# Performance work log

Hardware: AMD Instinct MI355X
Metric: run time of the kernel (lower is better)

The kernel has to match this reference:

```python
import jax, jax.numpy as jnp
import numpy as np

N_NODES = 100000
N_EDGES = 600000
N_GRAPHS = 64
DIM_IN = 128


def setup_inputs() -> dict:
    key = jax.random.key(0)
    ks = jax.random.split(key, 12)
    s = 0.05
    return {
        "feat": jax.random.normal(ks[0], (N_NODES, DIM_IN), jnp.float32),
        "Wself1": jax.random.normal(ks[1], (DIM_IN, 100), jnp.float32) * s,
        "Wneigh1": jax.random.normal(ks[2], (DIM_IN, 100), jnp.float32) * s,
        "b1": jnp.zeros((100,), jnp.float32),
        "Wself2": jax.random.normal(ks[3], (100, 20), jnp.float32) * s,
        "Wneigh2": jax.random.normal(ks[4], (100, 20), jnp.float32) * s,
        "b2": jnp.zeros((20,), jnp.float32),
        "fc1_w": jax.random.normal(ks[5], (20, 10), jnp.float32) * s,
        "fc1_b": jnp.zeros((10,), jnp.float32),
        "fc2_w": jax.random.normal(ks[6], (10, 1), jnp.float32) * s,
        "fc2_b": jnp.zeros((1,), jnp.float32),
        "src": jax.random.randint(ks[7], (N_EDGES,), 0, N_NODES, jnp.int32),
        "dst": jax.random.randint(ks[8], (N_EDGES,), 0, N_NODES, jnp.int32),
        "graph_ids": jnp.sort(jax.random.randint(ks[9], (N_NODES,), 0, N_GRAPHS, jnp.int32)),
    }


def _sage_mean(x, src, dst, inv_deg, Wself, Wneigh, b):
    # DGL SAGEConv(aggr='mean'): fc_self(h) + fc_neigh(mean of in-neighbor feats)
    msg = x[src]  # [E, d] gather
    agg = jax.ops.segment_sum(msg, dst, num_segments=N_NODES) * inv_deg  # [N, d]
    return x @ Wself + agg @ Wneigh + b


def reference(feat, Wself1, Wneigh1, b1, Wself2, Wneigh2, b2,
              fc1_w, fc1_b, fc2_w, fc2_b, src, dst, graph_ids):
    ones_e = jnp.ones((src.shape[0],), feat.dtype)
    deg = jax.ops.segment_sum(ones_e, dst, num_segments=N_NODES)
    inv_deg = (1.0 / jnp.maximum(deg, 1.0))[:, None]  # zero in-degree -> agg stays 0

    h = jax.nn.relu(_sage_mean(feat, src, dst, inv_deg, Wself1, Wneigh1, b1))
    h = jax.nn.relu(_sage_mean(h, src, dst, inv_deg, Wself2, Wneigh2, b2))

    # dgl.mean_nodes: per-graph mean over nodes
    ones_n = jnp.ones((h.shape[0],), h.dtype)
    counts = jax.ops.segment_sum(ones_n, graph_ids, num_segments=N_GRAPHS)
    hg = jax.ops.segment_sum(h, graph_ids, num_segments=N_GRAPHS) / jnp.maximum(counts, 1.0)[:, None]

    out = jax.nn.relu(hg @ fc1_w + fc1_b) @ fc2_w + fc2_b  # [G, 1]
    return out
```

## Files before the change

kernel.cpp:

```cpp
#include <hip/hip_runtime.h>
#include <cstddef>

#define N_NODES  100000
#define N_EDGES  600000
#define N_GRAPHS 64

__device__ __forceinline__ void atomAddF(float* p, float v) {
    unsafeAtomicAdd(p, v);
}

typedef __attribute__((address_space(1))) void GV;
typedef __attribute__((address_space(3))) void LV;
__device__ __forceinline__ void gload16(const float* g, float* l) {
    __builtin_amdgcn_global_load_lds((GV*)g, (LV*)l, 16, 0, 0);
}

__global__ __launch_bounds__(256) void deg_count(const int* __restrict__ dst,
                                                 int* __restrict__ deg) {
    int e = blockIdx.x * 256 + threadIdx.x;
    if (e < N_EDGES) atomicAdd(deg + dst[e], 1);
}

__global__ __launch_bounds__(256)
void alloc_ranges(const int* __restrict__ deg, int* __restrict__ beg,
                  int* __restrict__ cur, int* __restrict__ counter) {
    int n = blockIdx.x * 256 + threadIdx.x;
    int d = (n < N_NODES) ? deg[n] : 0;
    int lane = threadIdx.x & 63, wid = threadIdx.x >> 6;
    int incl = d;
#pragma unroll
    for (int o = 1; o < 64; o <<= 1) {
        int v = __shfl_up(incl, o);
        if (lane >= o) incl += v;
    }
    __shared__ int wsum[4];
    __shared__ int blockBase;
    if (lane == 63) wsum[wid] = incl;
    __syncthreads();
    if (threadIdx.x == 0) {
        int tot = wsum[0] + wsum[1] + wsum[2] + wsum[3];
        blockBase = atomicAdd(counter, tot);
    }
    __syncthreads();
    int base = blockBase;
    for (int w = 0; w < wid; ++w) base += wsum[w];
    int start = base + incl - d;
    if (n < N_NODES) { beg[n] = start; cur[n] = start; }
}

__global__ __launch_bounds__(256)
void csr_fill(const int* __restrict__ src, const int* __restrict__ dst,
              int* __restrict__ cur, int* __restrict__ csr_src) {
    int e = blockIdx.x * 256 + threadIdx.x;
    if (e >= N_EDGES) return;
    int p = atomicAdd(cur + dst[e], 1);
    csr_src[p] = src[e];
}

__global__ __launch_bounds__(256, 6)
void gemm1(const float* __restrict__ feat, const float* __restrict__ Wself,
           const float* __restrict__ Wneigh,
           float* __restrict__ S1, float* __restrict__ N1) {
    __shared__ float As[40 * 16];
    __shared__ float Bs[16][200];
    const int tid  = threadIdx.x;
    const int m0   = blockIdx.x * 40;
    const int wave = tid >> 6;
    const int lane = tid & 63;
    const bool active = tid < 250;
    const int tr  = tid / 25;
    const int tcc = tid % 25;
    const int sw  = tr & 3;

    float4 acc0[4], acc1[4];
#pragma unroll
    for (int i = 0; i < 4; ++i) {
        acc0[i] = make_float4(0.f, 0.f, 0.f, 0.f);
        acc1[i] = make_float4(0.f, 0.f, 0.f, 0.f);
    }

    for (int kt = 0; kt < 8; ++kt) {
        const int k0 = kt * 16;
        if (kt) __syncthreads();

        if (lane < 40) {
            int u  = wave * 40 + lane;
            int r  = u >> 2;
            int k4 = (u & 3) ^ ((r >> 2) & 3);
            gload16(feat + (size_t)(m0 + r) * 128 + k0 + k4 * 4, &As[wave * 160]);
        }
        for (int idx = tid; idx < 800; idx += 256) {
            int k = idx / 50, n4 = idx % 50;
            int n = n4 * 4;
            int gk = k0 + k;
            float4 v;
            if (n < 100) v = *reinterpret_cast<const float4*>(Wself + gk * 100 + n);
            else         v = *reinterpret_cast<const float4*>(Wneigh + gk * 100 + (n - 100));
            *reinterpret_cast<float4*>(&Bs[k][n]) = v;
        }
        __syncthreads();

        if (active) {
            const int abase = tr * 64;
#pragma unroll 4
            for (int k = 0; k < 16; ++k) {
                const float4 b0 = *reinterpret_cast<const float4*>(&Bs[k][tcc * 4]);
                const float4 b1 = *reinterpret_cast<const float4*>(&Bs[k][100 + tcc * 4]);
                const int kc = ((k >> 2) ^ sw) * 4 + (k & 3);
#pragma unroll
                for (int i = 0; i < 4; ++i) {
                    const float a = As[abase + i * 16 + kc];
                    acc0[i].x = fmaf(a, b0.x, acc0[i].x);
                    acc0[i].y = fmaf(a, b0.y, acc0[i].y);
                    acc0[i].z = fmaf(a, b0.z, acc0[i].z);
                    acc0[i].w = fmaf(a, b0.w, acc0[i].w);
                    acc1[i].x = fmaf(a, b1.x, acc1[i].x);
                    acc1[i].y = fmaf(a, b1.y, acc1[i].y);
                    acc1[i].z = fmaf(a, b1.z, acc1[i].z);
                    acc1[i].w = fmaf(a, b1.w, acc1[i].w);
                }
            }
        }
    }

    if (active) {
        const int c = tcc * 4;
#pragma unroll
        for (int i = 0; i < 4; ++i) {
            int gr = m0 + tr * 4 + i;
            *reinterpret_cast<float4*>(S1 + (size_t)gr * 100 + c) = acc0[i];
            *reinterpret_cast<float4*>(N1 + (size_t)gr * 100 + c) = acc1[i];
        }
    }
}

__global__ __launch_bounds__(256)
void aggregate1(const float* __restrict__ N1, const int* __restrict__ csr_src,
                const int* __restrict__ beg, const int* __restrict__ cur,
                float* __restrict__ A1) {
    int n  = blockIdx.x * 8 + (threadIdx.x >> 5);
    int c4 = threadIdx.x & 31;
    if (n >= N_NODES || c4 >= 25) return;
    int b = beg[n], end = cur[n];
    float4 acc = make_float4(0.f, 0.f, 0.f, 0.f);
    int j = b;
    for (; j + 1 < end; j += 2) {
        int s0 = csr_src[j], s1 = csr_src[j + 1];
        float4 v0 = *reinterpret_cast<const float4*>(N1 + (size_t)s0 * 100 + c4 * 4);
        float4 v1 = *reinterpret_cast<const float4*>(N1 + (size_t)s1 * 100 + c4 * 4);
        acc.x += v0.x + v1.x; acc.y += v0.y + v1.y;
        acc.z += v0.z + v1.z; acc.w += v0.w + v1.w;
    }
    if (j < end) {
        int s = csr_src[j];
        float4 v = *reinterpret_cast<const float4*>(N1 + (size_t)s * 100 + c4 * 4);
        acc.x += v.x; acc.y += v.y; acc.z += v.z; acc.w += v.w;
    }
    *reinterpret_cast<float4*>(A1 + (size_t)n * 100 + c4 * 4) = acc;
}

__global__ __launch_bounds__(256)
void gemm2(const float* __restrict__ S1, const float* __restrict__ A1,
           const int* __restrict__ deg, const float* __restrict__ b1,
           const float* __restrict__ Ws2, const float* __restrict__ Wn2,
           float* __restrict__ S2, float* __restrict__ N2) {
    __shared__ float As[64][108];
    __shared__ float Bs[100][64];
    const int tid = threadIdx.x;
    const int m0  = blockIdx.x * 64;

    for (int idx = tid; idx < 100 * 16; idx += 256) {
        int k = idx >> 4, n4 = idx & 15;
        int n = n4 * 4;
        float4 v = make_float4(0.f, 0.f, 0.f, 0.f);
        if (n < 20)       v = *reinterpret_cast<const float4*>(Ws2 + k * 20 + n);
        else if (n < 40)  v = *reinterpret_cast<const float4*>(Wn2 + k * 20 + (n - 20));
        *reinterpret_cast<float4*>(&Bs[k][n]) = v;
    }
    for (int idx = tid; idx < 64 * 25; idx += 256) {
        int r = idx / 25, k4 = idx % 25;
        int gr = m0 + r;
        float4 h = make_float4(0.f, 0.f, 0.f, 0.f);
        if (gr < N_NODES) {
            float4 s  = *reinterpret_cast<const float4*>(S1 + (size_t)gr * 100 + k4 * 4);
            float4 a  = *reinterpret_cast<const float4*>(A1 + (size_t)gr * 100 + k4 * 4);
            float4 bb = *reinterpret_cast<const float4*>(b1 + k4 * 4);
            float inv = 1.0f / (float)max(deg[gr], 1);
            h.x = fmaxf(fmaf(a.x, inv, s.x) + bb.x, 0.f);
            h.y = fmaxf(fmaf(a.y, inv, s.y) + bb.y, 0.f);
            h.z = fmaxf(fmaf(a.z, inv, s.z) + bb.z, 0.f);
            h.w = fmaxf(fmaf(a.w, inv, s.w) + bb.w, 0.f);
        }
        *reinterpret_cast<float4*>(&As[r][k4 * 4]) = h;
    }
    __syncthreads();

    const int tr = tid >> 4, tc = tid & 15;
    float acc[4][4] = {};
#pragma unroll 4
    for (int k = 0; k < 100; ++k) {
        float a0 = As[tr * 4 + 0][k];
        float a1 = As[tr * 4 + 1][k];
        float a2 = As[tr * 4 + 2][k];
        float a3 = As[tr * 4 + 3][k];
        float4 b = *reinterpret_cast<const float4*>(&Bs[k][tc * 4]);
        acc[0][0] += a0 * b.x; acc[0][1] += a0 * b.y; acc[0][2] += a0 * b.z; acc[0][3] += a0 * b.w;
        acc[1][0] += a1 * b.x; acc[1][1] += a1 * b.y; acc[1][2] += a1 * b.z; acc[1][3] += a1 * b.w;
        acc[2][0] += a2 * b.x; acc[2][1] += a2 * b.y; acc[2][2] += a2 * b.z; acc[2][3] += a2 * b.w;
        acc[3][0] += a3 * b.x; acc[3][1] += a3 * b.y; acc[3][2] += a3 * b.z; acc[3][3] += a3 * b.w;
    }

#pragma unroll
    for (int i = 0; i < 4; ++i) {
        int gr = m0 + tr * 4 + i;
        if (gr >= N_NODES) continue;
        int n = tc * 4;
        float4 v = make_float4(acc[i][0], acc[i][1], acc[i][2], acc[i][3]);
        if (n < 20)       *reinterpret_cast<float4*>(S2 + (size_t)gr * 20 + n) = v;
        else if (n < 40)  *reinterpret_cast<float4*>(N2 + (size_t)gr * 20 + (n - 20)) = v;
    }
}

__global__ __launch_bounds__(256)
void aggregate2(const float* __restrict__ N2, const int* __restrict__ csr_src,
                const int* __restrict__ beg, const int* __restrict__ cur,
                float* __restrict__ A2) {
    int n  = blockIdx.x * 32 + (threadIdx.x >> 3);
    int c4 = threadIdx.x & 7;
    if (n >= N_NODES || c4 >= 5) return;
    int b = beg[n], end = cur[n];
    float4 acc = make_float4(0.f, 0.f, 0.f, 0.f);
    int j = b;
    for (; j + 1 < end; j += 2) {
        int s0 = csr_src[j], s1 = csr_src[j + 1];
        float4 v0 = *reinterpret_cast<const float4*>(N2 + (size_t)s0 * 20 + c4 * 4);
        float4 v1 = *reinterpret_cast<const float4*>(N2 + (size_t)s1 * 20 + c4 * 4);
        acc.x += v0.x + v1.x; acc.y += v0.y + v1.y;
        acc.z += v0.z + v1.z; acc.w += v0.w + v1.w;
    }
    if (j < end) {
        int s = csr_src[j];
        float4 v = *reinterpret_cast<const float4*>(N2 + (size_t)s * 20 + c4 * 4);
        acc.x += v.x; acc.y += v.y; acc.z += v.z; acc.w += v.w;
    }
    *reinterpret_cast<float4*>(A2 + (size_t)n * 20 + c4 * 4) = acc;
}

__global__ __launch_bounds__(256)
void pool_kernel(const float* __restrict__ S2, const float* __restrict__ A2,
                 const int* __restrict__ deg, const float* __restrict__ b2,
                 const int* __restrict__ gids,
                 float* __restrict__ pool, float* __restrict__ cnt) {
    int n = blockIdx.x * 256 + threadIdx.x;
    float h[20];
    int g = -1;
    if (n < N_NODES) {
        g = gids[n];
        float inv = 1.0f / (float)max(deg[n], 1);
#pragma unroll
        for (int q = 0; q < 5; ++q) {
            float4 s = *reinterpret_cast<const float4*>(S2 + (size_t)n * 20 + q * 4);
            float4 a = *reinterpret_cast<const float4*>(A2 + (size_t)n * 20 + q * 4);
            float4 bb = *reinterpret_cast<const float4*>(b2 + q * 4);
            h[q * 4 + 0] = fmaxf(fmaf(a.x, inv, s.x) + bb.x, 0.f);
            h[q * 4 + 1] = fmaxf(fmaf(a.y, inv, s.y) + bb.y, 0.f);
            h[q * 4 + 2] = fmaxf(fmaf(a.z, inv, s.z) + bb.z, 0.f);
            h[q * 4 + 3] = fmaxf(fmaf(a.w, inv, s.w) + bb.w, 0.f);
        }
    } else {
#pragma unroll
        for (int c = 0; c < 20; ++c) h[c] = 0.f;
    }
    unsigned long long act = __ballot(n < N_NODES);
    int gfirst = __shfl(g, 0);
    bool uniform = __all(g == gfirst);
    if (uniform) {
        if (gfirst >= 0) {
#pragma unroll
            for (int c = 0; c < 20; ++c)
                for (int off2 = 32; off2 > 0; off2 >>= 1)
                    h[c] += __shfl_down(h[c], off2);
            if ((threadIdx.x & 63) == 0) {
                for (int c = 0; c < 20; ++c) atomAddF(&pool[gfirst * 20 + c], h[c]);
                atomAddF(&cnt[gfirst], (float)__popcll(act));
            }
        }
    } else if (n < N_NODES) {
        for (int c = 0; c < 20; ++c) atomAddF(&pool[g * 20 + c], h[c]);
        atomAddF(&cnt[g], 1.0f);
    }
}

__global__ __launch_bounds__(64)
void head(const float* __restrict__ pool, const float* __restrict__ cnt,
          const float* __restrict__ fc1w, const float* __restrict__ fc1b,
          const float* __restrict__ fc2w, const float* __restrict__ fc2b,
          float* __restrict__ out) {
    int g = threadIdx.x;
    if (g >= N_GRAPHS) return;
    float inv = 1.0f / fmaxf(cnt[g], 1.0f);
    float hg[20];
    for (int c = 0; c < 20; ++c) hg[c] = pool[g * 20 + c] * inv;
    float o = fc2b[0];
    for (int j = 0; j < 10; ++j) {
        float t = fc1b[j];
        for (int c = 0; c < 20; ++c) t = fmaf(hg[c], fc1w[c * 10 + j], t);
        o = fmaf(fmaxf(t, 0.f), fc2w[j], o);
    }
    out[g] = o;
}

extern "C" void kernel_launch(void* const* d_in, const int* in_sizes, int n_in,
                              void* d_out, int out_size, void* d_ws, size_t ws_size,
                              hipStream_t stream) {
    const float* feat   = (const float*)d_in[0];
    const float* Wself1 = (const float*)d_in[1];
    const float* Wneigh1= (const float*)d_in[2];
    const float* b1     = (const float*)d_in[3];
    const float* Wself2 = (const float*)d_in[4];
    const float* Wneigh2= (const float*)d_in[5];
    const float* b2     = (const float*)d_in[6];
    const float* fc1w   = (const float*)d_in[7];
    const float* fc1b   = (const float*)d_in[8];
    const float* fc2w   = (const float*)d_in[9];
    const float* fc2b   = (const float*)d_in[10];
    const int*   src    = (const int*)d_in[11];
    const int*   dst    = (const int*)d_in[12];
    const int*   gids   = (const int*)d_in[13];
    float* ws = (float*)d_ws;

    float* S1 = ws;
    float* N1 = ws + 10000000;
    float* A1 = ws + 20000000;
    float* S2 = N1;
    float* N2 = N1 + 2000000;
    float* A2 = A1;
    int*   deg  = (int*)(ws + 30000000);
    float* pool = ws + 30100000;
    float* cnt  = ws + 30101280;
    int*   ctr  = (int*)(ws + 30101344);
    int*   beg  = (int*)(ws + 30101360);
    int*   cur  = (int*)(ws + 30201360);
    int*   csr  = (int*)(ws + 30301360);

    hipMemsetAsync(deg, 0, (100000 + 1280 + 64 + 16) * sizeof(float), stream);

    deg_count<<<(N_EDGES + 255) / 256, 256, 0, stream>>>(dst, deg);
    alloc_ranges<<<(N_NODES + 255) / 256, 256, 0, stream>>>(deg, beg, cur, ctr);
    csr_fill<<<(N_EDGES + 255) / 256, 256, 0, stream>>>(src, dst, cur, csr);

    gemm1<<<N_NODES / 40, 256, 0, stream>>>(feat, Wself1, Wneigh1, S1, N1);

    aggregate1<<<(N_NODES + 7) / 8, 256, 0, stream>>>(N1, csr, beg, cur, A1);

    gemm2<<<(N_NODES + 63) / 64, 256, 0, stream>>>(S1, A1, deg, b1, Wself2, Wneigh2, S2, N2);

    aggregate2<<<(N_NODES + 31) / 32, 256, 0, stream>>>(N2, csr, beg, cur, A2);

    pool_kernel<<<(N_NODES + 255) / 256, 256, 0, stream>>>(S2, A2, deg, b2, gids, pool, cnt);

    head<<<1, 64, 0, stream>>>(pool, cnt, fc1w, fc1b, fc2w, fc2b, (float*)d_out);
}
```

Measured before the change: 303.7 us.

## Fuse bias/ReLU epilogue into aggregation kernels and vectorize GEMM A-reads

Moves the mean-normalize, self-term add, bias and ReLU from gemm2 and pool_kernel into aggregate1 and aggregate2. The aggregators now write final activations h1/h2, so gemm2 reads one 100-wide array instead of S1, A1 and deg. gemm2 loads its A tile with direct global-to-LDS loads, keeps only the 40 used output columns, and idles the other threads. gemm1's inner loop now reads A with float4 LDS loads, and h2 aliases S1 to reuse workspace.

After: 296.3 us. -2.4%, faster.

```diff
diff --git a/kernel.cpp b/kernel.cpp
--- a/kernel.cpp
+++ b/kernel.cpp
@@ -7,6 +7,10 @@
 
 __device__ __forceinline__ void atomAddF(float* p, float v) {
     unsafeAtomicAdd(p, v);
+}
+
+__device__ __forceinline__ float f4get(const float4& v, int i) {
+    return i == 0 ? v.x : i == 1 ? v.y : i == 2 ? v.z : v.w;
 }
 
 typedef __attribute__((address_space(1))) void GV;
@@ -102,22 +106,36 @@
 
         if (active) {
             const int abase = tr * 64;
-#pragma unroll 4
-            for (int k = 0; k < 16; ++k) {
-                const float4 b0 = *reinterpret_cast<const float4*>(&Bs[k][tcc * 4]);
-                const float4 b1 = *reinterpret_cast<const float4*>(&Bs[k][100 + tcc * 4]);
-                const int kc = ((k >> 2) ^ sw) * 4 + (k & 3);
-#pragma unroll
-                for (int i = 0; i < 4; ++i) {
-                    const float a = As[abase + i * 16 + kc];
-                    acc0[i].x = fmaf(a, b0.x, acc0[i].x);
-                    acc0[i].y = fmaf(a, b0.y, acc0[i].y);
-                    acc0[i].z = fmaf(a, b0.z, acc0[i].z);
-                    acc0[i].w = fmaf(a, b0.w, acc0[i].w);
-                    acc1[i].x = fmaf(a, b1.x, acc1[i].x);
-                    acc1[i].y = fmaf(a, b1.y, acc1[i].y);
-                    acc1[i].z = fmaf(a, b1.z, acc1[i].z);
-                    acc1[i].w = fmaf(a, b1.w, acc1[i].w);
+#pragma unroll
+            for (int g = 0; g < 4; ++g) {
+                const int ac = ((g ^ sw) << 2);
+                const float4 a0 = *reinterpret_cast<const float4*>(&As[abase +  0 + ac]);
+                const float4 a1 = *reinterpret_cast<const float4*>(&As[abase + 16 + ac]);
+                const float4 a2 = *reinterpret_cast<const float4*>(&As[abase + 32 + ac]);
+                const float4 a3 = *reinterpret_cast<const float4*>(&As[abase + 48 + ac]);
+#pragma unroll
+                for (int kl = 0; kl < 4; ++kl) {
+                    const int k = g * 4 + kl;
+                    const float4 b0 = *reinterpret_cast<const float4*>(&Bs[k][tcc * 4]);
+                    const float4 b1 = *reinterpret_cast<const float4*>(&Bs[k][100 + tcc * 4]);
+                    const float v0 = f4get(a0, kl), v1 = f4get(a1, kl);
+                    const float v2 = f4get(a2, kl), v3 = f4get(a3, kl);
+                    acc0[0].x = fmaf(v0, b0.x, acc0[0].x); acc0[0].y = fmaf(v0, b0.y, acc0[0].y);
+                    acc0[0].z = fmaf(v0, b0.z, acc0[0].z); acc0[0].w = fmaf(v0, b0.w, acc0[0].w);
+                    acc1[0].x = fmaf(v0, b1.x, acc1[0].x); acc1[0].y = fmaf(v0, b1.y, acc1[0].y);
+                    acc1[0].z = fmaf(v0, b1.z, acc1[0].z); acc1[0].w = fmaf(v0, b1.w, acc1[0].w);
+                    acc0[1].x = fmaf(v1, b0.x, acc0[1].x); acc0[1].y = fmaf(v1, b0.y, acc0[1].y);
+                    acc0[1].z = fmaf(v1, b0.z, acc0[1].z); acc0[1].w = fmaf(v1, b0.w, acc0[1].w);
+                    acc1[1].x = fmaf(v1, b1.x, acc1[1].x); acc1[1].y = fmaf(v1, b1.y, acc1[1].y);
+                    acc1[1].z = fmaf(v1, b1.z, acc1[1].z); acc1[1].w = fmaf(v1, b1.w, acc1[1].w);
+                    acc0[2].x = fmaf(v2, b0.x, acc0[2].x); acc0[2].y = fmaf(v2, b0.y, acc0[2].y);
+                    acc0[2].z = fmaf(v2, b0.z, acc0[2].z); acc0[2].w = fmaf(v2, b0.w, acc0[2].w);
+                    acc1[2].x = fmaf(v2, b1.x, acc1[2].x); acc1[2].y = fmaf(v2, b1.y, acc1[2].y);
+                    acc1[2].z = fmaf(v2, b1.z, acc1[2].z); acc1[2].w = fmaf(v2, b1.w, acc1[2].w);
+                    acc0[3].x = fmaf(v3, b0.x, acc0[3].x); acc0[3].y = fmaf(v3, b0.y, acc0[3].y);
+                    acc0[3].z = fmaf(v3, b0.z, acc0[3].z); acc0[3].w = fmaf(v3, b0.w, acc0[3].w);
+                    acc1[3].x = fmaf(v3, b1.x, acc1[3].x); acc1[3].y = fmaf(v3, b1.y, acc1[3].y);
+                    acc1[3].z = fmaf(v3, b1.z, acc1[3].z); acc1[3].w = fmaf(v3, b1.w, acc1[3].w);
                 }
             }
         }
@@ -135,9 +153,10 @@
 }
 
 __global__ __launch_bounds__(256)
-void aggregate1(const float* __restrict__ N1, const int* __restrict__ csr_src,
+void aggregate1(const float* __restrict__ N1, const float* __restrict__ S1,
+                const float* __restrict__ b1, const int* __restrict__ csr_src,
                 const int* __restrict__ beg, const int* __restrict__ cur,
-                float* __restrict__ A1) {
+                float* __restrict__ h1) {
     int n  = blockIdx.x * 8 + (threadIdx.x >> 5);
     int c4 = threadIdx.x & 31;
     if (n >= N_NODES || c4 >= 25) return;
@@ -156,75 +175,80 @@
         float4 v = *reinterpret_cast<const float4*>(N1 + (size_t)s * 100 + c4 * 4);
         acc.x += v.x; acc.y += v.y; acc.z += v.z; acc.w += v.w;
     }
-    *reinterpret_cast<float4*>(A1 + (size_t)n * 100 + c4 * 4) = acc;
-}
-
-__global__ __launch_bounds__(256)
-void gemm2(const float* __restrict__ S1, const float* __restrict__ A1,
-           const int* __restrict__ deg, const float* __restrict__ b1,
+    float inv = 1.0f / (float)max(end - b, 1);
+    float4 s  = *reinterpret_cast<const float4*>(S1 + (size_t)n * 100 + c4 * 4);
+    float4 bb = *reinterpret_cast<const float4*>(b1 + c4 * 4);
+    float4 h;
+    h.x = fmaxf(fmaf(acc.x, inv, s.x) + bb.x, 0.f);
+    h.y = fmaxf(fmaf(acc.y, inv, s.y) + bb.y, 0.f);
+    h.z = fmaxf(fmaf(acc.z, inv, s.z) + bb.z, 0.f);
+    h.w = fmaxf(fmaf(acc.w, inv, s.w) + bb.w, 0.f);
+    *reinterpret_cast<float4*>(h1 + (size_t)n * 100 + c4 * 4) = h;
+}
+
+__global__ __launch_bounds__(256)
+void gemm2(const float* __restrict__ h1,
            const float* __restrict__ Ws2, const float* __restrict__ Wn2,
            float* __restrict__ S2, float* __restrict__ N2) {
-    __shared__ float As[64][108];
-    __shared__ float Bs[100][64];
-    const int tid = threadIdx.x;
-    const int m0  = blockIdx.x * 64;
-
-    for (int idx = tid; idx < 100 * 16; idx += 256) {
-        int k = idx >> 4, n4 = idx & 15;
+    __shared__ float As[64 * 100];
+    __shared__ float Bs[100][40];
+    const int tid  = threadIdx.x;
+    const int m0   = blockIdx.x * 64;
+    const int wave = tid >> 6;
+    const int lane = tid & 63;
+
+#pragma unroll
+    for (int t = 0; t < 7; ++t) {
+        int u0 = t * 256 + wave * 64;
+        if (u0 < 1600) {
+            int u  = u0 + lane;
+            int r  = u / 25, c4 = u % 25;
+            int gr = m0 + r; if (gr >= N_NODES) gr = N_NODES - 1;
+            gload16(h1 + (size_t)gr * 100 + c4 * 4, &As[u0 * 4]);
+        }
+    }
+    for (int idx = tid; idx < 1000; idx += 256) {
+        int k = idx / 10, n4 = idx % 10;
         int n = n4 * 4;
-        float4 v = make_float4(0.f, 0.f, 0.f, 0.f);
-        if (n < 20)       v = *reinterpret_cast<const float4*>(Ws2 + k * 20 + n);
-        else if (n < 40)  v = *reinterpret_cast<const float4*>(Wn2 + k * 20 + (n - 20));
+        float4 v;
+        if (n < 20) v = *reinterpret_cast<const float4*>(Ws2 + k * 20 + n);
+        else        v = *reinterpret_cast<const float4*>(Wn2 + k * 20 + (n - 20));
         *reinterpret_cast<float4*>(&Bs[k][n]) = v;
     }
-    for (int idx = tid; idx < 64 * 25; idx += 256) {
-        int r = idx / 25, k4 = idx % 25;
-        int gr = m0 + r;
-        float4 h = make_float4(0.f, 0.f, 0.f, 0.f);
-        if (gr < N_NODES) {
-            float4 s  = *reinterpret_cast<const float4*>(S1 + (size_t)gr * 100 + k4 * 4);
-            float4 a  = *reinterpret_cast<const float4*>(A1 + (size_t)gr * 100 + k4 * 4);
-            float4 bb = *reinterpret_cast<const float4*>(b1 + k4 * 4);
-            float inv = 1.0f / (float)max(deg[gr], 1);
-            h.x = fmaxf(fmaf(a.x, inv, s.x) + bb.x, 0.f);
-            h.y = fmaxf(fmaf(a.y, inv, s.y) + bb.y, 0.f);
-            h.z = fmaxf(fmaf(a.z, inv, s.z) + bb.z, 0.f);
-            h.w = fmaxf(fmaf(a.w, inv, s.w) + bb.w, 0.f);
-        }
-        *reinterpret_cast<float4*>(&As[r][k4 * 4]) = h;
-    }
     __syncthreads();
 
     const int tr = tid >> 4, tc = tid & 15;
-    float acc[4][4] = {};
+    if (tc < 10) {
+        float acc[4][4] = {};
 #pragma unroll 4
-    for (int k = 0; k < 100; ++k) {
-        float a0 = As[tr * 4 + 0][k];
-        float a1 = As[tr * 4 + 1][k];
-        float a2 = As[tr * 4 + 2][k];
-        float a3 = As[tr * 4 + 3][k];
-        float4 b = *reinterpret_cast<const float4*>(&Bs[k][tc * 4]);
-        acc[0][0] += a0 * b.x; acc[0][1] += a0 * b.y; acc[0][2] += a0 * b.z; acc[0][3] += a0 * b.w;
-        acc[1][0] += a1 * b.x; acc[1][1] += a1 * b.y; acc[1][2] += a1 * b.z; acc[1][3] += a1 * b.w;
-        acc[2][0] += a2 * b.x; acc[2][1] += a2 * b.y; acc[2][2] += a2 * b.z; acc[2][3] += a2 * b.w;
-        acc[3][0] += a3 * b.x; acc[3][1] += a3 * b.y; acc[3][2] += a3 * b.z; acc[3][3] += a3 * b.w;
-    }
-
-#pragma unroll
-    for (int i = 0; i < 4; ++i) {
-        int gr = m0 + tr * 4 + i;
-        if (gr >= N_NODES) continue;
-        int n = tc * 4;
-        float4 v = make_float4(acc[i][0], acc[i][1], acc[i][2], acc[i][3]);
-        if (n < 20)       *reinterpret_cast<float4*>(S2 + (size_t)gr * 20 + n) = v;
-        else if (n < 40)  *reinterpret_cast<float4*>(N2 + (size_t)gr * 20 + (n - 20)) = v;
-    }
-}
-
-__global__ __launch_bounds__(256)
-void aggregate2(const float* __restrict__ N2, const int* __restrict__ csr_src,
+        for (int k = 0; k < 100; ++k) {
+            float a0 = As[(tr * 4 + 0) * 100 + k];
+            float a1 = As[(tr * 4 + 1) * 100 + k];
+            float a2 = As[(tr * 4 + 2) * 100 + k];
+            float a3 = As[(tr * 4 + 3) * 100 + k];
+            float4 b = *reinterpret_cast<const float4*>(&Bs[k][tc * 4]);
+            acc[0][0] += a0 * b.x; acc[0][1] += a0 * b.y; acc[0][2] += a0 * b.z; acc[0][3] += a0 * b.w;
+            acc[1][0] += a1 * b.x; acc[1][1] += a1 * b.y; acc[1][2] += a1 * b.z; acc[1][3] += a1 * b.w;
+            acc[2][0] += a2 * b.x; acc[2][1] += a2 * b.y; acc[2][2] += a2 * b.z; acc[2][3] += a2 * b.w;
+            acc[3][0] += a3 * b.x; acc[3][1] += a3 * b.y; acc[3][2] += a3 * b.z; acc[3][3] += a3 * b.w;
+        }
+#pragma unroll
+        for (int i = 0; i < 4; ++i) {
+            int gr = m0 + tr * 4 + i;
+            if (gr >= N_NODES) continue;
+            int n = tc * 4;
+            float4 v = make_float4(acc[i][0], acc[i][1], acc[i][2], acc[i][3]);
+            if (n < 20) *reinterpret_cast<float4*>(S2 + (size_t)gr * 20 + n) = v;
+            else        *reinterpret_cast<float4*>(N2 + (size_t)gr * 20 + (n - 20)) = v;
+        }
+    }
+}
+
+__global__ __launch_bounds__(256)
+void aggregate2(const float* __restrict__ N2, const float* __restrict__ S2,
+                const float* __restrict__ b2, const int* __restrict__ csr_src,
                 const int* __restrict__ beg, const int* __restrict__ cur,
-                float* __restrict__ A2) {
+                float* __restrict__ h2) {
     int n  = blockIdx.x * 32 + (threadIdx.x >> 3);
     int c4 = threadIdx.x & 7;
     if (n >= N_NODES || c4 >= 5) return;
@@ -243,29 +267,30 @@
         float4 v = *reinterpret_cast<const float4*>(N2 + (size_t)s * 20 + c4 * 4);
         acc.x += v.x; acc.y += v.y; acc.z += v.z; acc.w += v.w;
     }
-    *reinterpret_cast<float4*>(A2 + (size_t)n * 20 + c4 * 4) = acc;
-}
-
-__global__ __launch_bounds__(256)
-void pool_kernel(const float* __restrict__ S2, const float* __restrict__ A2,
-                 const int* __restrict__ deg, const float* __restrict__ b2,
-                 const int* __restrict__ gids,
+    float inv = 1.0f / (float)max(end - b, 1);
+    float4 s  = *reinterpret_cast<const float4*>(S2 + (size_t)n * 20 + c4 * 4);
+    float4 bb = *reinterpret_cast<const float4*>(b2 + c4 * 4);
+    float4 h;
+    h.x = fmaxf(fmaf(acc.x, inv, s.x) + bb.x, 0.f);
+    h.y = fmaxf(fmaf(acc.y, inv, s.y) + bb.y, 0.f);
+    h.z = fmaxf(fmaf(acc.z, inv, s.z) + bb.z, 0.f);
+    h.w = fmaxf(fmaf(acc.w, inv, s.w) + bb.w, 0.f);
+    *reinterpret_cast<float4*>(h2 + (size_t)n * 20 + c4 * 4) = h;
+}
+
+__global__ __launch_bounds__(256)
+void pool_kernel(const float* __restrict__ h2, const int* __restrict__ gids,
                  float* __restrict__ pool, float* __restrict__ cnt) {
     int n = blockIdx.x * 256 + threadIdx.x;
     float h[20];
     int g = -1;
     if (n < N_NODES) {
         g = gids[n];
-        float inv = 1.0f / (float)max(deg[n], 1);
 #pragma unroll
         for (int q = 0; q < 5; ++q) {
-            float4 s = *reinterpret_cast<const float4*>(S2 + (size_t)n * 20 + q * 4);
-            float4 a = *reinterpret_cast<const float4*>(A2 + (size_t)n * 20 + q * 4);
-            float4 bb = *reinterpret_cast<const float4*>(b2 + q * 4);
-            h[q * 4 + 0] = fmaxf(fmaf(a.x, inv, s.x) + bb.x, 0.f);
-            h[q * 4 + 1] = fmaxf(fmaf(a.y, inv, s.y) + bb.y, 0.f);
-            h[q * 4 + 2] = fmaxf(fmaf(a.z, inv, s.z) + bb.z, 0.f);
-            h[q * 4 + 3] = fmaxf(fmaf(a.w, inv, s.w) + bb.w, 0.f);
+            float4 v = *reinterpret_cast<const float4*>(h2 + (size_t)n * 20 + q * 4);
+            h[q * 4 + 0] = v.x; h[q * 4 + 1] = v.y;
+            h[q * 4 + 2] = v.z; h[q * 4 + 3] = v.w;
         }
     } else {
 #pragma unroll
@@ -331,10 +356,10 @@
 
     float* S1 = ws;
     float* N1 = ws + 10000000;
-    float* A1 = ws + 20000000;
+    float* h1 = ws + 20000000;
     float* S2 = N1;
     float* N2 = N1 + 2000000;
-    float* A2 = A1;
+    float* h2 = S1;
     int*   deg  = (int*)(ws + 30000000);
     float* pool = ws + 30100000;
     float* cnt  = ws + 30101280;
@@ -351,13 +376,13 @@
 
     gemm1<<<N_NODES / 40, 256, 0, stream>>>(feat, Wself1, Wneigh1, S1, N1);
 
-    aggregate1<<<(N_NODES + 7) / 8, 256, 0, stream>>>(N1, csr, beg, cur, A1);
-
-    gemm2<<<(N_NODES + 63) / 64, 256, 0, stream>>>(S1, A1, deg, b1, Wself2, Wneigh2, S2, N2);
-
-    aggregate2<<<(N_NODES + 31) / 32, 256, 0, stream>>>(N2, csr, beg, cur, A2);
-
-    pool_kernel<<<(N_NODES + 255) / 256, 256, 0, stream>>>(S2, A2, deg, b2, gids, pool, cnt);
+    aggregate1<<<(N_NODES + 7) / 8, 256, 0, stream>>>(N1, S1, b1, csr, beg, cur, h1);
+
+    gemm2<<<(N_NODES + 63) / 64, 256, 0, stream>>>(h1, Wself2, Wneigh2, S2, N2);
+
+    aggregate2<<<(N_NODES + 31) / 32, 256, 0, stream>>>(N2, S2, b2, csr, beg, cur, h2);
+
+    pool_kernel<<<(N_NODES + 255) / 256, 256, 0, stream>>>(h2, gids, pool, cnt);
 
     head<<<1, 64, 0, stream>>>(pool, cnt, fc1w, fc1b, fc2w, fc2b, (float*)d_out);
 }
```
